# Performance work log

Measured on AMD Instinct MI355X. Metric: run time of the kernel, lower is better.

Reference implementation:

```python
import math
import jax, jax.numpy as jnp
import numpy as np

B = 32            # batch
C = 64            # prior_feat_channels == fc_hidden_dim
MID = 48          # ROIGather mid_channels
P = 192           # num_priors
S = 36            # sample_points
N_OFFSETS = 72
N_STRIPS = 71
IMG_W, IMG_H = 800, 320
SCALE_FACTOR = 20.0
RH, RW = 10, 25   # FeatureResize target size

SAMPLE_X_IDX = np.floor(np.linspace(0.0, 1.0, S) * N_STRIPS).astype(np.int32)
PRIOR_FEAT_YS = (1.0 - SAMPLE_X_IDX.astype(np.float32) / N_STRIPS)[::-1].copy()
PRIOR_YS = np.linspace(1.0, 0.0, N_OFFSETS, dtype=np.float32)
SX = jnp.asarray(SAMPLE_X_IDX)

def _make_priors():
    pri = np.zeros((P, 6 + N_OFFSETS), np.float32)
    pri[:, 0], pri[:, 1], pri[:, 2] = 0.1, 0.9, 0.5
    pri[:, 3], pri[:, 4], pri[:, 5] = 0.1, 0.0, 50.0
    pri[:, 6:] = ((np.arange(P, dtype=np.float32) + 0.5) / P)[:, None]
    return jnp.asarray(pri)

def _conv1d(x, w, pad):
    # x (N, Cin, L), w (Cout, Cin, K); cross-correlation like torch
    return jax.lax.conv_general_dilated(x, w, (1,), [(pad, pad)], dimension_numbers=('NCH', 'OIH', 'NCH'))

def _resize_nearest(x):
    # F.interpolate(mode='nearest') to (RH, RW), then flatten(2)
    b, c, h, w = x.shape
    hi = (jnp.arange(RH) * h) // RH
    wi = (jnp.arange(RW) * w) // RW
    return x[:, :, hi[:, None], wi[None, :]].reshape(b, c, RH * RW)

def _grid_sample(feat, gx, gy):
    # bilinear, align_corners=True, zeros padding; feat (B,C,H,W), gx/gy (B,P,S)
    b, c, h, w = feat.shape
    ix = (gx + 1.0) * 0.5 * (w - 1)
    iy = (gy + 1.0) * 0.5 * (h - 1)
    x0, y0 = jnp.floor(ix), jnp.floor(iy)
    fflat = feat.reshape(b, c, h * w)
    def corner(xc, yc, wt):
        valid = (xc >= 0) & (xc <= w - 1) & (yc >= 0) & (yc <= h - 1)
        xi = jnp.clip(xc, 0, w - 1).astype(jnp.int32)
        yi = jnp.clip(yc, 0, h - 1).astype(jnp.int32)
        idx = (yi * w + xi).reshape(b, 1, -1)
        v = jnp.take_along_axis(fflat, jnp.broadcast_to(idx, (b, c, idx.shape[-1])), axis=2)
        return v.reshape(b, c, *xc.shape[1:]) * (wt * valid)[:, None]
    return (corner(x0, y0, (x0 + 1 - ix) * (y0 + 1 - iy))
            + corner(x0 + 1, y0, (ix - x0) * (y0 + 1 - iy))
            + corner(x0, y0 + 1, (x0 + 1 - ix) * (iy - y0))
            + corner(x0 + 1, y0 + 1, (ix - x0) * (iy - y0)))


def setup_inputs() -> dict:
    key = jax.random.key(0)
    ks = iter(jax.random.split(key, 64))
    def rn(shape, s=0.05):
        return jax.random.normal(next(ks), shape, jnp.float32) * s
    def ru(shape):
        return jax.random.uniform(next(ks), shape, jnp.float32, 0.5, 1.5)
    return dict(
        feat_s8=rn((B, C, 40, 100), 1.0), feat_s16=rn((B, C, 20, 50), 1.0), feat_s32=rn((B, C, 10, 25), 1.0),
        rg_conv_w=rn((3, MID, C, 9)), rg_conv_scale=ru((3, MID)), rg_conv_bias=rn((3, MID)),
        catconv0_w=rn((C, MID, 9)), catconv1_w=rn((C, 2 * MID, 9)), catconv2_w=rn((C, 3 * MID, 9)),
        catconv_scale=ru((3, C)), catconv_bias=rn((3, C)),
        fc_w=rn((C, C * S)), fc_b=rn((C,)), ln_gamma=ru((C,)), ln_beta=rn((C,)),
        fkey_w=rn((C, C)), fkey_scale=ru((C,)), fkey_bias=rn((C,)),
        fvalue_w=rn((C, C)), fvalue_b=rn((C,)),
        fquery_w=ru((P,)), fquery_b=rn((P,)), attn_w_scale=rn((P,)), attn_w_bias=rn((P,)),
        cls_w1=rn((C, C)), cls_b1=rn((C,)), cls_w2=rn((C, C)), cls_b2=rn((C,)),
        reg_w1=rn((C, C)), reg_b1=rn((C,)), reg_w2=rn((C, C)), reg_b2=rn((C,)),
        cls_head_w=rn((2, C)), cls_head_b=rn((2,)),
        reg_head_w=rn((N_OFFSETS + 4, C)), reg_head_b=rn((N_OFFSETS + 4,)),
        cat_w1=rn((C, C)), cat_b1=rn((C,)), cat_w2=rn((C, C)), cat_b2=rn((C,)),
        prototypes=rn((15, C), 0.01),
        attr_w1=rn((C, C)), attr_b1=rn((C,)), attr_w2=rn((C, C)), attr_b2=rn((C,)),
        attr_head_w=rn((4, C)), attr_head_b=rn((4,)),
    )


def reference(feat_s8, feat_s16, feat_s32, rg_conv_w, rg_conv_scale, rg_conv_bias,
              catconv0_w, catconv1_w, catconv2_w, catconv_scale, catconv_bias,
              fc_w, fc_b, ln_gamma, ln_beta, fkey_w, fkey_scale, fkey_bias,
              fvalue_w, fvalue_b, fquery_w, fquery_b, attn_w_scale, attn_w_bias,
              cls_w1, cls_b1, cls_w2, cls_b2, reg_w1, reg_b1, reg_w2, reg_b2,
              cls_head_w, cls_head_b, reg_head_w, reg_head_b,
              cat_w1, cat_b1, cat_w2, cat_b2, prototypes,
              attr_w1, attr_b1, attr_w2, attr_b2, attr_head_w, attr_head_b):
    relu = jax.nn.relu
    catconv_ws = (catconv0_w, catconv1_w, catconv2_w)
    batch_features = [feat_s32, feat_s16, feat_s8]  # features[-3:] reversed
    priors = jnp.broadcast_to(_make_priors()[None], (B, P, 6 + N_OFFSETS))
    pofm = priors[..., 6 + SX]
    prior_ys = jnp.asarray(PRIOR_YS)
    gy_row = jnp.asarray(PRIOR_FEAT_YS) * 2.0 - 1.0  # (S,)

    roi_stages, predictions, ff_last = [], None, None
    for stage in range(3):
        feat = batch_features[stage]
        prior_xs = jnp.flip(pofm, axis=2)            # (B,P,S)
        gx = prior_xs * 2.0 - 1.0
        gy = jnp.broadcast_to(gy_row[None, None, :], gx.shape)
        pooled = _grid_sample(feat, gx, gy)          # (B,C,P,S)
        pooled = pooled.transpose(0, 2, 1, 3).reshape(B * P, C, S)
        roi_stages.append(pooled)

        # ROIGather.roi_fea: per-stage (9,1) convs (BN folded to scale/bias) + cat conv
        feats = [relu(_conv1d(roi_stages[i], rg_conv_w[i], 4)
                      * rg_conv_scale[i][None, :, None] + rg_conv_bias[i][None, :, None])
                 for i in range(stage + 1)]
        cat_feat = jnp.concatenate(feats, axis=1)
        roi = relu(_conv1d(cat_feat, catconv_ws[stage], 4)
                   * catconv_scale[stage][None, :, None] + catconv_bias[stage][None, :, None])
        # fc + LayerNorm + relu
        roi = roi.reshape(B * P, C * S) @ fc_w.T + fc_b
        mu = roi.mean(-1, keepdims=True)
        var = ((roi - mu) ** 2).mean(-1, keepdims=True)
        roi = (roi - mu) * jax.lax.rsqrt(var + 1e-5) * ln_gamma + ln_beta
        roi = relu(roi).reshape(B, P, C)

        # cross-attention with (nearest-)resized feature map
        key_map = relu(jnp.einsum('bchw,oc->bohw', feat, fkey_w)
                       * fkey_scale[None, :, None, None] + fkey_bias[None, :, None, None])
        key_map = _resize_nearest(key_map)                     # (B,C,N)
        val_map = jnp.einsum('bchw,oc->bohw', feat, fvalue_w) + fvalue_b[None, :, None, None]
        val_map = _resize_nearest(val_map).transpose(0, 2, 1)  # (B,N,C)
        query = relu(roi * fquery_w[None, :, None] + fquery_b[None, :, None])  # grouped 1x1 conv1d
        sim = jax.nn.softmax(jnp.einsum('bpc,bcn->bpn', query, key_map) * (C ** -0.5), axis=-1)
        context = jnp.einsum('bpn,bnc->bpc', sim, val_map)
        context = context * attn_w_scale[None, :, None] + attn_w_bias[None, :, None]
        roi = roi + context

        # faithful to source: view(P,B,C).permute(1,0,2) memory reinterpretation
        ff = roi.reshape(P, B, C).transpose(1, 0, 2).reshape(B * P, C)
        ff_last = ff

        cls_f = relu(ff @ cls_w1.T + cls_b1)
        cls_f = relu(cls_f @ cls_w2.T + cls_b2)
        reg_f = relu(ff @ reg_w1.T + reg_b1)
        reg_f = relu(reg_f @ reg_w2.T + reg_b2)
        cls_logits = (cls_f @ cls_head_w.T + cls_head_b).reshape(B, P, 2)
        reg = (reg_f @ reg_head_w.T + reg_head_b).reshape(B, P, N_OFFSETS + 4)

        p2 = priors[:, :, 2] + reg[:, :, 0]
        p3 = priors[:, :, 3] + reg[:, :, 1]
        p4 = priors[:, :, 4] + reg[:, :, 2]
        p5 = reg[:, :, 3]
        geom = (p3[:, :, None] * (IMG_W - 1)
                + (1.0 - prior_ys[None, None, :] - p2[:, :, None]) * IMG_H
                / jnp.tan(p4[:, :, None] * math.pi + 1e-5)) / (IMG_W - 1)
        lines = jnp.concatenate([cls_logits, p2[..., None], p3[..., None],
                                 p4[..., None], p5[..., None], geom], axis=-1)
        predictions = lines.at[..., 6:].add(reg[:, :, 4:])
        if stage != 2:
            priors = jax.lax.stop_gradient(lines)
            pofm = priors[..., 6 + SX]

    # prototype-based cosine category head (final stage features)
    cat_f = relu(ff_last @ cat_w1.T + cat_b1)
    cat_f = relu(cat_f @ cat_w2.T + cat_b2)
    cat_n = cat_f / jnp.maximum(jnp.linalg.norm(cat_f, axis=-1, keepdims=True), 1e-12)
    proto_n = prototypes / jnp.maximum(jnp.linalg.norm(prototypes, axis=-1, keepdims=True), 1e-12)
    category = (cat_n @ proto_n.T * SCALE_FACTOR).reshape(B, P, -1)
    # left-right attribute head
    attr_f = relu(ff_last @ attr_w1.T + attr_b1)
    attr_f = relu(attr_f @ attr_w2.T + attr_b2)
    attribute = (attr_f @ attr_head_w.T + attr_head_b).reshape(B, P, -1)
    return predictions, category, attribute
```

## Files before the change

kernel.cpp:

```cpp
#include <hip/hip_runtime.h>
#include <math.h>

#define PPRI 192
#define NB   32
#define NS   36
#define BP   6144
#define NPIX 250
#define FPI  3.14159265358979323846f

typedef _Float16 f16x8 __attribute__((ext_vector_type(8)));
typedef float f32x4  __attribute__((ext_vector_type(4)));

__device__ inline short f2h(float x) {
    _Float16 h = (_Float16)x;
    return *(short*)&h;
}
__device__ inline float h2f(short s) {
    _Float16 h = *(_Float16*)&s;
    return (float)h;
}
__device__ inline void splith(float x, short& h, short& l) {
    h = f2h(x); l = f2h(x - h2f(h));
}

// ... 14 lines not shown
                       const float* __restrict__ attr_w1, const float* __restrict__ attr_w2,
                       const float* __restrict__ reg_head_w, const float* __restrict__ cls_head_w,
                       const float* __restrict__ attr_head_w) {
    int i = blockIdx.x * 256 + threadIdx.x;
    if (i < BP * NS) {
        int p = (i / NS) % PPRI;
        pofm[i] = ((float)p + 0.5f) / 192.0f;
    }
    if (i < BP) {
        p234[3*i+0] = 0.5f; p234[3*i+1] = 0.1f; p234[3*i+2] = 0.0f;
    }
    if (i < 64 * 2304) {
        int o = i / 2304, k = i % 2304;
        int s = k >> 6, oc = k & 63;
        short h, l; splith(fc_w[o * 2304 + oc * 36 + s], h, l);
        fcBh[i] = h; fcBl[i] = l;
    }
    if (i < 82944) {
        int st = i / 27648, r = i % 27648;
        int k = r / 3072, r2 = r % 3072;
        int oc = r2 / 64, ic = r2 & 63;
        short h, l; splith(rg_w[((st*48 + oc)*64 + ic)*9 + k], h, l);
        rgWh[i] = h; rgWl[i] = l;
    }
    if (i < 184320) {
        int st, base, icw; const float* w;
        if (i < 36864)      { st = 0; base = 0;     icw = 64;  w = cw0; }
        else if (i < 92160) { st = 1; base = 36864; icw = 96;  w = cw1; }
        else                { st = 2; base = 92160; icw = 160; w = cw2; }
        int r = i - base;
        int k = r / (64*icw), r2 = r % (64*icw);
        int oc = r2 / icw, icp = r2 % icw;
        int IC = 48 * (st + 1);
        float wv = (icp < IC) ? w[(oc*IC + icp)*9 + k] : 0.f;
        short h, l; splith(wv, h, l);
        catWh[i] = h; catWl[i] = l;
    }
    if (i < 32768) {
        int m = i >> 12, r2 = i & 4095, c = r2 >> 6, o = r2 & 63;
        const float* Ws[8] = {reg_w1, reg_w2, cls_w1, cls_w2, cat_w1, cat_w2, attr_w1, attr_w2};
        hT[i] = Ws[m][o*64 + c];
    }
    if (i < 76*64) {
        int c = i / 76, o = i % 76;
        rhwT[c*76 + o] = reg_head_w[o*64 + c];
    }
    if (i < 128) {
        int c = i >> 1, o = i & 1;
        chwT[c*2 + o] = cls_head_w[o*64 + c];
    }
    if (i < 256) {
        int c = i >> 2, o = i & 3;
        ahwT[c*4 + o] = attr_head_w[o*64 + c];
    }
    if (i < 960) {
        int c = i / 15, p = i % 15;
        float ss = 0.f;
        for (int j = 0; j < 64; ++j) { float v = protos[p*64 + j]; ss += v*v; }
        float nrm = fmaxf(sqrtf(ss), 1e-12f);
        protoNT[c*15 + p] = protos[p*64 + c] / nrm;
    }
}

__global__ __launch_bounds__(256) void k_transpose(const float* __restrict__ in,
                                                   float* __restrict__ outT, int HW) {
    __shared__ float t[64][65];
    int b = blockIdx.y;
    int hw0 = blockIdx.x * 64;
    int tx = threadIdx.x & 63, ty = threadIdx.x >> 6;
    const float* ib = in + (size_t)b * 64 * HW;
    for (int c = ty; c < 64; c += 4) {
        int hw = hw0 + tx;
        t[c][tx] = (hw < HW) ? ib[(size_t)c * HW + hw] : 0.f;
    }
    __syncthreads();
    float* ob = outT + (size_t)b * HW * 64;
    for (int r = ty; r < 64; r += 4) {
        int hw = hw0 + r;
        if (hw < HW) ob[(size_t)hw * 64 + tx] = t[tx][r];
    }
}

#define RGWP 80
template<bool SPL>
__global__ __launch_bounds__(192) void k_rgfused(
        const float* __restrict__ featT, int H, int W,
        const float* __restrict__ pofm,
        const short* __restrict__ Wh, const short* __restrict__ Wl,
        const float* __restrict__ scale, const float* __restrict__ bias,
        short* __restrict__ outH, short* __restrict__ outL) {
    constexpr int STG = (SPL ? 2 : 1) * 37 * RGWP;
    constexpr int RED = 9 * 256 * 2;
    constexpr int SMS = (STG > RED) ? STG : RED;
    __shared__ short sm[SMS];
    int tid = threadIdx.x;
    int row = blockIdx.x;
    int wv = tid >> 6, lane = tid & 63;
    int b = row / PPRI;
    float myPof = (lane < 36) ? pofm[row * 36 + lane] : 0.f;
    const float* fb = featT + (size_t)b * H * W * 64;
    for (int si = 0; si < 12; ++si) {
        int s = wv * 12 + si;
        float px = __shfl(myPof, 35 - s);
        px = fminf(fmaxf(px, -1e6f), 1e6f);
        float pfy = (s == 0) ? 0.0f : ((float)(2*s+1) / 71.0f);
        float ix = px  * (float)(W - 1);
        float iy = pfy * (float)(H - 1);
        float x0f = floorf(ix), y0f = floorf(iy);
        float fx = ix - x0f, fy = iy - y0f;
        float vx0 = (x0f >= 0.f     && x0f     <= (float)(W-1)) ? 1.f : 0.f;
        float vx1 = (x0f+1.f >= 0.f && x0f+1.f <= (float)(W-1)) ? 1.f : 0.f;
        float vy0 = (y0f >= 0.f     && y0f     <= (float)(H-1)) ? 1.f : 0.f;
        float vy1 = (y0f+1.f >= 0.f && y0f+1.f <= (float)(H-1)) ? 1.f : 0.f;
        int x0 = min(max((int)x0f, 0), W-1);
        int x1 = min(max((int)x0f + 1, 0), W-1);
        int y0 = min(max((int)y0f, 0), H-1);
        int y1 = min(max((int)y0f + 1, 0), H-1);
        float w00 = (1.f-fx)*(1.f-fy)*vx0*vy0, w10 = fx*(1.f-fy)*vx1*vy0;
        float w01 = (1.f-fx)*fy*vx0*vy1,       w11 = fx*fy*vx1*vy1;
        float v = w00 * fb[(size_t)(y0*W+x0)*64 + lane]
                + w10 * fb[(size_t)(y0*W+x1)*64 + lane]
                + w01 * fb[(size_t)(y1*W+x0)*64 + lane]
                + w11 * fb[(size_t)(y1*W+x1)*64 + lane];
        int di = (s*RGWP + lane) ^ (((s >> 2) & 1) << 3);
        if (SPL) {
            short h, l; splith(v, h, l);
            sm[di] = h;
            sm[37*RGWP + di] = l;
        } else {
            sm[di] = f2h(v);
        }
    }
    if (wv == 0) {
        int di = (36*RGWP + lane) ^ 8;
        sm[di] = 0;
        if (SPL) sm[37*RGWP + di] = 0;
    }
    __syncthreads();
    int lr = lane & 15, kg = lane >> 4;
    const short* shb = sm;
    const short* slb = sm + 37*RGWP;
    f32x4 acc[3][3] = {};
    #pragma unroll
    for (int ssh = 0; ssh < 3; ++ssh) {
        int sh = wv*3 + ssh;
        int sr0 = lr + sh - 4;
        int ar0 = ((unsigned)sr0 < 36u) ? sr0 : 36;
        int ar1 = 16 + lr + sh - 4;
        int sr2 = 32 + lr + sh - 4;
        int ar2 = ((unsigned)sr2 < 36u) ? sr2 : 36;
        int rb0 = ar0*RGWP, rs0 = ((ar0 >> 2) & 1) << 3;
        int rb1 = ar1*RGWP, rs1 = ((ar1 >> 2) & 1) << 3;
        int rb2 = ar2*RGWP, rs2 = ((ar2 >> 2) & 1) << 3;
        #pragma unroll
        for (int kc = 0; kc < 2; ++kc) {
            int icb = kc*32 + kg*8;
            int d0 = (rb0 + icb) ^ rs0;
            int d1 = (rb1 + icb) ^ rs1;
            int d2 = (rb2 + icb) ^ rs2;
            f16x8 ah[3] = { *(const f16x8*)(shb + d0), *(const f16x8*)(shb + d1),
                            *(const f16x8*)(shb + d2) };
            const short* wbh = Wh + (size_t)(sh*48)*64 + icb;
            f16x8 bh[3];
            #pragma unroll
            for (int nt = 0; nt < 3; ++nt) bh[nt] = *(const f16x8*)(wbh + (nt*16 + lr)*64);
            if (SPL) {
                f16x8 al[3] = { *(const f16x8*)(slb + d0), *(const f16x8*)(slb + d1),
                                *(const f16x8*)(slb + d2) };
                const short* wbl = Wl + (size_t)(sh*48)*64 + icb;
                f16x8 bl[3];
                #pragma unroll
                for (int nt = 0; nt < 3; ++nt) bl[nt] = *(const f16x8*)(wbl + (nt*16 + lr)*64);
                #pragma unroll
                for (int nt = 0; nt < 3; ++nt)
                    #pragma unroll
                    for (int mt = 0; mt < 3; ++mt)
                        acc[mt][nt] = __builtin_amdgcn_mfma_f32_16x16x32_f16(ah[mt], bh[nt], acc[mt][nt], 0,0,0);
                #pragma unroll
                for (int nt = 0; nt < 3; ++nt)
                    #pragma unroll
                    for (int mt = 0; mt < 3; ++mt)
                        acc[mt][nt] = __builtin_amdgcn_mfma_f32_16x16x32_f16(ah[mt], bl[nt], acc[mt][nt], 0,0,0);
                #pragma unroll
                for (int nt = 0; nt < 3; ++nt)
                    #pragma unroll
                    for (int mt = 0; mt < 3; ++mt)
                        acc[mt][nt] = __builtin_amdgcn_mfma_f32_16x16x32_f16(al[mt], bh[nt], acc[mt][nt], 0,0,0);
            } else {
                #pragma unroll
                for (int nt = 0; nt < 3; ++nt)
                    #pragma unroll
                    for (int mt = 0; mt < 3; ++mt)
                        acc[mt][nt] = __builtin_amdgcn_mfma_f32_16x16x32_f16(ah[mt], bh[nt], acc[mt][nt], 0,0,0);
            }
        }
    }
    __syncthreads();
    float* red = (float*)sm;
    if (wv == 2) {
        #pragma unroll
        for (int mt = 0; mt < 3; ++mt)
            #pragma unroll
            for (int nt = 0; nt < 3; ++nt)
                *(f32x4*)(red + ((size_t)(mt*3 + nt))*256 + lane*4) = acc[mt][nt];
    }
    __syncthreads();
    if (wv == 1) {
        #pragma unroll
        for (int mt = 0; mt < 3; ++mt)
            #pragma unroll
            for (int nt = 0; nt < 3; ++nt) {
                f32x4* p = (f32x4*)(red + ((size_t)(mt*3 + nt))*256 + lane*4);
                *p = *p + acc[mt][nt];
            }
    }
    __syncthreads();
    if (wv == 0) {
        #pragma unroll
        for (int nt = 0; nt < 3; ++nt) {
            int oc = nt*16 + lr;
            float sc = scale[oc], bi = bias[oc];
            #pragma unroll
            for (int mt = 0; mt < 3; ++mt) {
                f32x4 a = acc[mt][nt] + *(const f32x4*)(red + ((size_t)(mt*3 + nt))*256 + lane*4);
                #pragma unroll
                for (int i = 0; i < 4; ++i) {
                    int s = mt*16 + kg*4 + i;
                    if (s < 36) {
                        float v = fmaxf(a[i]*sc + bi, 0.f);
                        if (SPL) {
                            short h, l; splith(v, h, l);
                            outH[(size_t)row*36*48 + s*48 + oc] = h;
                            outL[(size_t)row*36*48 + s*48 + oc] = l;
                        } else {
                            outH[(size_t)row*36*48 + s*48 + oc] = f2h(v);
                        }
                    }
                }
            }
        }
    }
}

template<int NC, int NT, int BW, int WP, int ICR, bool SPL>
__global__ __launch_bounds__(192) void k_catconv(
        const short* __restrict__ Xh, const short* __restrict__ Xl,
        const short* __restrict__ Wh, const short* __restrict__ Wl,
        const float* __restrict__ scale, const float* __restrict__ bias,
        short* __restrict__ outH, short* __restrict__ outL) {
    constexpr int icw = NC * 32;
    constexpr int CH  = icw / 8;
    constexpr int STG = (SPL ? 2 : 1) * 37 * WP;
    constexpr int RED = 3 * NT * 256 * 2;
    constexpr int SMS = (STG > RED) ? STG : RED;
    __shared__ short sm[SMS];
    int tid = threadIdx.x;
    int row = blockIdx.x;
    for (int idx = tid; idx < 37*CH; idx += 192) {
        int pos = idx / CH, c0 = (idx % CH) << 3;
        f16x8 h = {}, l = {};
        if (pos < 36 && c0 < ICR) {
            int sidx = c0 / BW, cc = c0 % BW;
            size_t src = ((size_t)(sidx*BP + row)*36 + pos)*BW + cc;
            h = *(const f16x8*)(Xh + src);
            if (SPL) l = *(const f16x8*)(Xl + src);
        }
        int di = (pos*WP + c0) ^ (((pos >> 2) & 1) << 3);
        *(f16x8*)(sm + di) = h;
        if (SPL) *(f16x8*)(sm + 37*WP + di) = l;
    }
    __syncthreads();
    int wv = tid >> 6, lane = tid & 63;
    int lr = lane & 15, kg = lane >> 4;
    const short* shb = sm;
    const short* slb = sm + 37*WP;
    f32x4 acc[3][NT] = {};
    #pragma unroll
    for (int ssh = 0; ssh < 3; ++ssh) {
        int sh = wv*3 + ssh;
        int sr0 = lr + sh - 4;
        int ar0 = ((unsigned)sr0 < 36u) ? sr0 : 36;
        int ar1 = 16 + lr + sh - 4;
        int sr2 = 32 + lr + sh - 4;
        int ar2 = ((unsigned)sr2 < 36u) ? sr2 : 36;
        int rb0 = ar0*WP, rs0 = ((ar0 >> 2) & 1) << 3;
        int rb1 = ar1*WP, rs1 = ((ar1 >> 2) & 1) << 3;
        int rb2 = ar2*WP, rs2 = ((ar2 >> 2) & 1) << 3;
        #pragma unroll
        for (int kc = 0; kc < NC; ++kc) {
            int icb = kc*32 + kg*8;
            int d0 = (rb0 + icb) ^ rs0;
            int d1 = (rb1 + icb) ^ rs1;
            int d2 = (rb2 + icb) ^ rs2;
            f16x8 ah[3] = { *(const f16x8*)(shb + d0), *(const f16x8*)(shb + d1),
                            *(const f16x8*)(shb + d2) };
            const short* wbh = Wh + (size_t)(sh*NT*16)*icw + icb;
            f16x8 bh[NT];
            #pragma unroll
            for (int nt = 0; nt < NT; ++nt) bh[nt] = *(const f16x8*)(wbh + (nt*16 + lr)*icw);
            if (SPL) {
                f16x8 al[3] = { *(const f16x8*)(slb + d0), *(const f16x8*)(slb + d1),
                                *(const f16x8*)(slb + d2) };
                const short* wbl = Wl + (size_t)(sh*NT*16)*icw + icb;
                f16x8 bl[NT];
                #pragma unroll
                for (int nt = 0; nt < NT; ++nt) bl[nt] = *(const f16x8*)(wbl + (nt*16 + lr)*icw);
                #pragma unroll
                for (int nt = 0; nt < NT; ++nt)
                    #pragma unroll
                    for (int mt = 0; mt < 3; ++mt)
                        acc[mt][nt] = __builtin_amdgcn_mfma_f32_16x16x32_f16(ah[mt], bh[nt], acc[mt][nt], 0,0,0);
                #pragma unroll
                for (int nt = 0; nt < NT; ++nt)
                    #pragma unroll
                    for (int mt = 0; mt < 3; ++mt)
                        acc[mt][nt] = __builtin_amdgcn_mfma_f32_16x16x32_f16(ah[mt], bl[nt], acc[mt][nt], 0,0,0);
                #pragma unroll
                for (int nt = 0; nt < NT; ++nt)
                    #pragma unroll
                    for (int mt = 0; mt < 3; ++mt)
                        acc[mt][nt] = __builtin_amdgcn_mfma_f32_16x16x32_f16(al[mt], bh[nt], acc[mt][nt], 0,0,0);
            } else {
                #pragma unroll
                for (int nt = 0; nt < NT; ++nt)
                    #pragma unroll
                    for (int mt = 0; mt < 3; ++mt)
                        acc[mt][nt] = __builtin_amdgcn_mfma_f32_16x16x32_f16(ah[mt], bh[nt], acc[mt][nt], 0,0,0);
            }
        }
    }
    __syncthreads();
    float* red = (float*)sm;
    if (wv == 2) {
        #pragma unroll
        for (int mt = 0; mt < 3; ++mt)
            #pragma unroll
            for (int nt = 0; nt < NT; ++nt)
                *(f32x4*)(red + ((size_t)(mt*NT + nt))*256 + lane*4) = acc[mt][nt];
    }
    __syncthreads();
    if (wv == 1) {
        #pragma unroll
        for (int mt = 0; mt < 3; ++mt)
            #pragma unroll
            for (int nt = 0; nt < NT; ++nt) {
                f32x4* p = (f32x4*)(red + ((size_t)(mt*NT + nt))*256 + lane*4);
                *p = *p + acc[mt][nt];
            }
    }
    __syncthreads();
    if (wv == 0) {
        constexpr int OC = NT * 16;
        #pragma unroll
        for (int nt = 0; nt < NT; ++nt) {
            int oc = nt*16 + lr;
            float sc = scale[oc], bi = bias[oc];
            #pragma unroll
            for (int mt = 0; mt < 3; ++mt) {
                f32x4 a = acc[mt][nt] + *(const f32x4*)(red + ((size_t)(mt*NT + nt))*256 + lane*4);
                #pragma unroll
                for (int i = 0; i < 4; ++i) {
                    int s = mt*16 + kg*4 + i;
                    if (s < 36) {
                        float v = fmaxf(a[i]*sc + bi, 0.f);
                        short h, l; splith(v, h, l);
                        outH[(size_t)row*36*OC + s*OC + oc] = h;
                        outL[(size_t)row*36*OC + s*OC + oc] = l;
                    }
                }
            }
        }
    }
}

__global__ __launch_bounds__(256) void k_fc_mfma(
        const short* __restrict__ Ah, const short* __restrict__ Al,
        const short* __restrict__ Bh, const short* __restrict__ Bl,
        const float* __restrict__ fcb,
        const float* __restrict__ gamma, const float* __restrict__ beta,
        float* __restrict__ roi) {
    __shared__ float red[3 * 4 * 256];
    __shared__ float lnb[16][65];
    int tid = threadIdx.x;
    int wv = tid >> 6, lane = tid & 63;
    int lr = lane & 15, kg = lane >> 4;
    int row0 = blockIdx.x * 16;
    f32x4 acc[4] = {};
    for (int kk = 0; kk < 18; ++kk) {
        int k = (wv*18 + kk)*32 + kg*8;
        size_t ar = (size_t)(row0 + lr)*2304 + k;
        f16x8 ah = *(const f16x8*)(Ah + ar);
        f16x8 al = *(const f16x8*)(Al + ar);
        f16x8 bh[4], bl[4];
        #pragma unroll
        for (int nt = 0; nt < 4; ++nt) {
            size_t br = (size_t)(nt*16 + lr)*2304 + k;
            bh[nt] = *(const f16x8*)(Bh + br);
            bl[nt] = *(const f16x8*)(Bl + br);
        }
        #pragma unroll
        for (int nt = 0; nt < 4; ++nt)
            acc[nt] = __builtin_amdgcn_mfma_f32_16x16x32_f16(ah, bh[nt], acc[nt], 0,0,0);
        #pragma unroll
        for (int nt = 0; nt < 4; ++nt)
            acc[nt] = __builtin_amdgcn_mfma_f32_16x16x32_f16(ah, bl[nt], acc[nt], 0,0,0);
        #pragma unroll
        for (int nt = 0; nt < 4; ++nt)
            acc[nt] = __builtin_amdgcn_mfma_f32_16x16x32_f16(al, bh[nt], acc[nt], 0,0,0);
    }
    if (wv > 0) {
        #pragma unroll
        for (int nt = 0; nt < 4; ++nt)
            *(f32x4*)(red + ((size_t)((wv-1)*4 + nt))*256 + lane*4) = acc[nt];
    }
    __syncthreads();
    if (wv == 0) {
        #pragma unroll
        for (int nt = 0; nt < 4; ++nt) {
            f32x4 a = acc[nt]
                    + *(const f32x4*)(red + ((size_t)(0*4 + nt))*256 + lane*4)
                    + *(const f32x4*)(red + ((size_t)(1*4 + nt))*256 + lane*4)
                    + *(const f32x4*)(red + ((size_t)(2*4 + nt))*256 + lane*4);
            #pragma unroll
            for (int i = 0; i < 4; ++i)
                lnb[kg*4 + i][nt*16 + lr] = a[i];
        }
    }
    __syncthreads();
    #pragma unroll
    for (int rr = 0; rr < 4; ++rr) {
        int r = wv*4 + rr;
        float y = lnb[r][lane] + fcb[lane];
        float sum = y;
        #pragma unroll
        for (int off = 32; off > 0; off >>= 1) sum += __shfl_xor(sum, off);
        float mu = sum * (1.f/64.f);
        float d = y - mu;
        float vs = d * d;
        #pragma unroll
        for (int off = 32; off > 0; off >>= 1) vs += __shfl_xor(vs, off);
        float var = vs * (1.f/64.f);
        float outv = d * (1.0f / sqrtf(var + 1e-5f)) * gamma[lane] + beta[lane];
        roi[(size_t)(row0 + r)*64 + lane] = fmaxf(outv, 0.f);
    }
}

__global__ __launch_bounds__(64) void k_keyval(const float* __restrict__ featT, int H, int W,
        const float* __restrict__ kw, const float* __restrict__ ks, const float* __restrict__ kb,
        const float* __restrict__ vw, const float* __restrict__ vb,
        float* __restrict__ keymap, float* __restrict__ valmap) {
// ... 193 lines not shown
    const float* rg_conv_w     = (const float*)d_in[3];
    const float* rg_conv_scale = (const float*)d_in[4];
    const float* rg_conv_bias  = (const float*)d_in[5];
    const float* catconv_w[3]  = {(const float*)d_in[6], (const float*)d_in[7], (const float*)d_in[8]};
    const float* catconv_scale = (const float*)d_in[9];
    const float* catconv_bias  = (const float*)d_in[10];
    const float* fc_w = (const float*)d_in[11];
    const float* fc_b = (const float*)d_in[12];
    const float* ln_gamma = (const float*)d_in[13];
    const float* ln_beta  = (const float*)d_in[14];
    const float* fkey_w = (const float*)d_in[15];
    const float* fkey_scale = (const float*)d_in[16];
    const float* fkey_bias  = (const float*)d_in[17];
    const float* fvalue_w = (const float*)d_in[18];
    const float* fvalue_b = (const float*)d_in[19];
    const float* fquery_w = (const float*)d_in[20];
    const float* fquery_b = (const float*)d_in[21];
    const float* attn_w_scale = (const float*)d_in[22];
    const float* attn_w_bias  = (const float*)d_in[23];
    const float* cls_w1 = (const float*)d_in[24];
    const float* cls_b1 = (const float*)d_in[25];
    const float* cls_w2 = (const float*)d_in[26];
    const float* cls_b2 = (const float*)d_in[27];
    const float* reg_w1 = (const float*)d_in[28];
    const float* reg_b1 = (const float*)d_in[29];
    const float* reg_w2 = (const float*)d_in[30];
    const float* reg_b2 = (const float*)d_in[31];
    const float* cls_head_w = (const float*)d_in[32];
    const float* cls_head_b = (const float*)d_in[33];
    const float* reg_head_w = (const float*)d_in[34];
    const float* reg_head_b = (const float*)d_in[35];
    const float* cat_w1 = (const float*)d_in[36];
    const float* cat_b1 = (const float*)d_in[37];
    const float* cat_w2 = (const float*)d_in[38];
    const float* cat_b2 = (const float*)d_in[39];
    const float* prototypes = (const float*)d_in[40];
    const float* attr_w1 = (const float*)d_in[41];
    const float* attr_b1 = (const float*)d_in[42];
    const float* attr_w2 = (const float*)d_in[43];
    const float* attr_b2 = (const float*)d_in[44];
    const float* attr_head_w = (const float*)d_in[45];
    const float* attr_head_b = (const float*)d_in[46];

    float* ws = (float*)d_ws;
    float* pofm   = ws;
    float* p234   = ws + 221184;
    short* fcBh   = (short*)(ws + 240576);
    short* fcBl   = (short*)(ws + 314304);
    float* roi    = ws + 388032;
    float* keymap = ws + 781248;
    float* valmap = ws + 1293248;
    short* catHh  = (short*)(ws + 1805248);
    short* catHl  = (short*)(ws + 8883136);
    float* featT  = ws + 15961024;
    short* rgCh   = (short*)(ws + 30116800);
    short* rgCl   = (short*)(ws + 46042048);
    short* rgWh   = (short*)(ws + 61967296);
    short* rgWl   = (short*)(ws + 62008768);
    short* catWh  = (short*)(ws + 62050240);
    short* catWl  = (short*)(ws + 62142400);
    float* hT      = ws + 62234560;
    float* rhwT    = ws + 62267328;
    float* chwT    = ws + 62272192;
    float* ahwT    = ws + 62272320;
    float* protoNT = ws + 62272576;

    float* out = (float*)d_out;

    k_init<<<864, 256, 0, stream>>>(pofm, p234, fcBh, fcBl, fc_w, prototypes,
                                    rgWh, rgWl, rg_conv_w, catWh, catWl,
                                    catconv_w[0], catconv_w[1], catconv_w[2],
                                    hT, rhwT, chwT, ahwT, protoNT,
                                    reg_w1, reg_w2, cls_w1, cls_w2,
                                    cat_w1, cat_w2, attr_w1, attr_w2,
                                    reg_head_w, cls_head_w, attr_head_w);

    const float* feats[3] = {feat_s32, feat_s16, feat_s8};
    const int Hs[3] = {10, 20, 40}, Wstg[3] = {25, 50, 100};
    const int catbase[3] = {0, 36864, 92160};

    for (int st = 0; st < 3; ++st) {
        int HW = Hs[st] * Wstg[st];
        k_transpose<<<dim3((HW + 63)/64, NB), 256, 0, stream>>>(feats[st], featT, HW);
        if (st < 2)
            k_rgfused<true><<<BP, 192, 0, stream>>>(featT, Hs[st], Wstg[st], pofm,
                                                    rgWh + st*27648, rgWl + st*27648,
                                                    rg_conv_scale + st*48, rg_conv_bias + st*48,
                                                    rgCh + (size_t)st*BP*1728, rgCl + (size_t)st*BP*1728);
        else
            k_rgfused<false><<<BP, 192, 0, stream>>>(featT, Hs[st], Wstg[st], pofm,
                                                     rgWh + st*27648, rgWl + st*27648,
                                                     rg_conv_scale + st*48, rg_conv_bias + st*48,
                                                     rgCh + (size_t)st*BP*1728, rgCl + (size_t)st*BP*1728);
        if (st == 0)
            k_catconv<2,4,48,80,48,true><<<BP, 192, 0, stream>>>(
                    rgCh, rgCl, catWh + catbase[0], catWl + catbase[0],
                    catconv_scale, catconv_bias, catHh, catHl);
        else if (st == 1)
            k_catconv<3,4,48,112,96,true><<<BP, 192, 0, stream>>>(
                    rgCh, rgCl, catWh + catbase[1], catWl + catbase[1],
                    catconv_scale + 64, catconv_bias + 64, catHh, catHl);
        else
            k_catconv<5,4,48,176,144,false><<<BP, 192, 0, stream>>>(
                    rgCh, rgCl, catWh + catbase[2], catWl + catbase[2],
                    catconv_scale + 128, catconv_bias + 128, catHh, catHl);
        k_fc_mfma<<<384, 256, 0, stream>>>(catHh, catHl, fcBh, fcBl,
                                           fc_b, ln_gamma, ln_beta, roi);
        k_keyval<<<NB*NPIX, 64, 0, stream>>>(featT, Hs[st], Wstg[st],
                                             fkey_w, fkey_scale, fkey_bias,
                                             fvalue_w, fvalue_b, keymap, valmap);
        k_attn<<<BP, 256, 0, stream>>>(roi, keymap, valmap, fquery_w, fquery_b,
                                       attn_w_scale, attn_w_bias);
        k_head<<<BP, 128, 0, stream>>>(st, p234, pofm, roi,
                                       hT + 0, reg_b1, hT + 4096, reg_b2, rhwT, reg_head_b,
                                       hT + 8192, cls_b1, hT + 12288, cls_b2, chwT, cls_head_b,
                                       out);
    }
    k_catattr<<<BP, 64, 0, stream>>>(roi, hT + 16384, cat_b1, hT + 20480, cat_b2, protoNT,
                                     hT + 24576, attr_b1, hT + 28672, attr_b2,
                                     ahwT, attr_head_b, out);
}
```

Baseline: 1.037 ms.

## Fuse ROI gather conv with concatenated stage conv in one kernel

Merges the per-stage gather-and-conv kernel with the following concatenation conv kernel, so each row's freshly computed gather features are written straight into the shared staging buffer of the second convolution. Only earlier stages' features are re-read from global memory, and the last stage no longer writes its gather output to global. This removes one launch per stage and a global round trip. In exchange shared memory use per block grows because separate buffers for both convolutions and the reduction now coexist, which may lower occupancy.

```diff
diff --git a/kernel.cpp b/kernel.cpp
--- a/kernel.cpp
+++ b/kernel.cpp
@@ -120,17 +120,25 @@
 }
 
 #define RGWP 80
-template<bool SPL>
-__global__ __launch_bounds__(192) void k_rgfused(
+template<int NC, int NT, int BW, int WP, int ICR, int OWN0, bool SPL, bool WRG>
+__global__ __launch_bounds__(192) void k_rgcat(
         const float* __restrict__ featT, int H, int W,
         const float* __restrict__ pofm,
-        const short* __restrict__ Wh, const short* __restrict__ Wl,
-        const float* __restrict__ scale, const float* __restrict__ bias,
+        const short* __restrict__ rWh, const short* __restrict__ rWl,
+        const float* __restrict__ rsc, const float* __restrict__ rbi,
+        const short* __restrict__ cWh, const short* __restrict__ cWl,
+        const float* __restrict__ csc, const float* __restrict__ cbi,
+        short* __restrict__ rgHout, short* __restrict__ rgLout,
+        const short* __restrict__ Xh, const short* __restrict__ Xl,
         short* __restrict__ outH, short* __restrict__ outL) {
-    constexpr int STG = (SPL ? 2 : 1) * 37 * RGWP;
-    constexpr int RED = 9 * 256 * 2;
-    constexpr int SMS = (STG > RED) ? STG : RED;
-    __shared__ short sm[SMS];
+    constexpr int icw  = NC * 32;
+    constexpr int CH   = icw / 8;
+    constexpr int ARW  = (SPL ? 2 : 1) * 37 * RGWP;
+    constexpr int BRW  = (SPL ? 2 : 1) * 37 * WP;
+    constexpr int REDS = (3*NT*512 > 9*512) ? 3*NT*512 : 9*512;
+    __shared__ short smA[ARW];
+    __shared__ short smB[BRW];
+    __shared__ short smR[REDS];
     int tid = threadIdx.x;
     int row = blockIdx.x;
     int wv = tid >> 6, lane = tid & 63;
@@ -163,139 +171,21 @@
         int di = (s*RGWP + lane) ^ (((s >> 2) & 1) << 3);
         if (SPL) {
             short h, l; splith(v, h, l);
-            sm[di] = h;
-            sm[37*RGWP + di] = l;
+            smA[di] = h;
+            smA[37*RGWP + di] = l;
         } else {
-            sm[di] = f2h(v);
+            smA[di] = f2h(v);
         }
     }
     if (wv == 0) {
         int di = (36*RGWP + lane) ^ 8;
-        sm[di] = 0;
-        if (SPL) sm[37*RGWP + di] = 0;
-    }
-    __syncthreads();
-    int lr = lane & 15, kg = lane >> 4;
-    const short* shb = sm;
-    const short* slb = sm + 37*RGWP;
-    f32x4 acc[3][3] = {};
-    #pragma unroll
-    for (int ssh = 0; ssh < 3; ++ssh) {
-        int sh = wv*3 + ssh;
-        int sr0 = lr + sh - 4;
-        int ar0 = ((unsigned)sr0 < 36u) ? sr0 : 36;
-        int ar1 = 16 + lr + sh - 4;
-        int sr2 = 32 + lr + sh - 4;
-        int ar2 = ((unsigned)sr2 < 36u) ? sr2 : 36;
-        int rb0 = ar0*RGWP, rs0 = ((ar0 >> 2) & 1) << 3;
-        int rb1 = ar1*RGWP, rs1 = ((ar1 >> 2) & 1) << 3;
-        int rb2 = ar2*RGWP, rs2 = ((ar2 >> 2) & 1) << 3;
-        #pragma unroll
-        for (int kc = 0; kc < 2; ++kc) {
-            int icb = kc*32 + kg*8;
-            int d0 = (rb0 + icb) ^ rs0;
-            int d1 = (rb1 + icb) ^ rs1;
-            int d2 = (rb2 + icb) ^ rs2;
-            f16x8 ah[3] = { *(const f16x8*)(shb + d0), *(const f16x8*)(shb + d1),
-                            *(const f16x8*)(shb + d2) };
-            const short* wbh = Wh + (size_t)(sh*48)*64 + icb;
-            f16x8 bh[3];
-            #pragma unroll
-            for (int nt = 0; nt < 3; ++nt) bh[nt] = *(const f16x8*)(wbh + (nt*16 + lr)*64);
-            if (SPL) {
-                f16x8 al[3] = { *(const f16x8*)(slb + d0), *(const f16x8*)(slb + d1),
-                                *(const f16x8*)(slb + d2) };
-                const short* wbl = Wl + (size_t)(sh*48)*64 + icb;
-                f16x8 bl[3];
-                #pragma unroll
-                for (int nt = 0; nt < 3; ++nt) bl[nt] = *(const f16x8*)(wbl + (nt*16 + lr)*64);
-                #pragma unroll
-                for (int nt = 0; nt < 3; ++nt)
-                    #pragma unroll
-                    for (int mt = 0; mt < 3; ++mt)
-                        acc[mt][nt] = __builtin_amdgcn_mfma_f32_16x16x32_f16(ah[mt], bh[nt], acc[mt][nt], 0,0,0);
-                #pragma unroll
-                for (int nt = 0; nt < 3; ++nt)
-                    #pragma unroll
-                    for (int mt = 0; mt < 3; ++mt)
-                        acc[mt][nt] = __builtin_amdgcn_mfma_f32_16x16x32_f16(ah[mt], bl[nt], acc[mt][nt], 0,0,0);
-                #pragma unroll
-                for (int nt = 0; nt < 3; ++nt)
-                    #pragma unroll
-                    for (int mt = 0; mt < 3; ++mt)
-                        acc[mt][nt] = __builtin_amdgcn_mfma_f32_16x16x32_f16(al[mt], bh[nt], acc[mt][nt], 0,0,0);
-            } else {
-                #pragma unroll
-                for (int nt = 0; nt < 3; ++nt)
-                    #pragma unroll
-                    for (int mt = 0; mt < 3; ++mt)
-                        acc[mt][nt] = __builtin_amdgcn_mfma_f32_16x16x32_f16(ah[mt], bh[nt], acc[mt][nt], 0,0,0);
-            }
-        }
-    }
-    __syncthreads();
-    float* red = (float*)sm;
-    if (wv == 2) {
-        #pragma unroll
-        for (int mt = 0; mt < 3; ++mt)
-            #pragma unroll
-            for (int nt = 0; nt < 3; ++nt)
-                *(f32x4*)(red + ((size_t)(mt*3 + nt))*256 + lane*4) = acc[mt][nt];
-    }
-    __syncthreads();
-    if (wv == 1) {
-        #pragma unroll
-        for (int mt = 0; mt < 3; ++mt)
-            #pragma unroll
-            for (int nt = 0; nt < 3; ++nt) {
-                f32x4* p = (f32x4*)(red + ((size_t)(mt*3 + nt))*256 + lane*4);
-                *p = *p + acc[mt][nt];
-            }
-    }
-    __syncthreads();
-    if (wv == 0) {
-        #pragma unroll
-        for (int nt = 0; nt < 3; ++nt) {
-            int oc = nt*16 + lr;
-            float sc = scale[oc], bi = bias[oc];
-            #pragma unroll
-            for (int mt = 0; mt < 3; ++mt) {
-                f32x4 a = acc[mt][nt] + *(const f32x4*)(red + ((size_t)(mt*3 + nt))*256 + lane*4);
-                #pragma unroll
-                for (int i = 0; i < 4; ++i) {
-                    int s = mt*16 + kg*4 + i;
-                    if (s < 36) {
-                        float v = fmaxf(a[i]*sc + bi, 0.f);
-                        if (SPL) {
-                            short h, l; splith(v, h, l);
-                            outH[(size_t)row*36*48 + s*48 + oc] = h;
-                            outL[(size_t)row*36*48 + s*48 + oc] = l;
-                        } else {
-                            outH[(size_t)row*36*48 + s*48 + oc] = f2h(v);
-                        }
-                    }
-                }
-            }
-        }
-    }
-}
-
-template<int NC, int NT, int BW, int WP, int ICR, bool SPL>
-__global__ __launch_bounds__(192) void k_catconv(
-        const short* __restrict__ Xh, const short* __restrict__ Xl,
-        const short* __restrict__ Wh, const short* __restrict__ Wl,
-        const float* __restrict__ scale, const float* __restrict__ bias,
-        short* __restrict__ outH, short* __restrict__ outL) {
-    constexpr int icw = NC * 32;
-    constexpr int CH  = icw / 8;
-    constexpr int STG = (SPL ? 2 : 1) * 37 * WP;
-    constexpr int RED = 3 * NT * 256 * 2;
-    constexpr int SMS = (STG > RED) ? STG : RED;
-    __shared__ short sm[SMS];
-    int tid = threadIdx.x;
-    int row = blockIdx.x;
+        smA[di] = 0;
+        if (SPL) smA[37*RGWP + di] = 0;
+    }
     for (int idx = tid; idx < 37*CH; idx += 192) {
         int pos = idx / CH, c0 = (idx % CH) << 3;
+        bool own = (c0 >= OWN0) && (c0 < OWN0 + 48);
+        if (own && pos < 36) continue;
         f16x8 h = {}, l = {};
         if (pos < 36 && c0 < ICR) {
             int sidx = c0 / BW, cc = c0 % BW;
@@ -304,106 +194,219 @@
             if (SPL) l = *(const f16x8*)(Xl + src);
         }
         int di = (pos*WP + c0) ^ (((pos >> 2) & 1) << 3);
-        *(f16x8*)(sm + di) = h;
-        if (SPL) *(f16x8*)(sm + 37*WP + di) = l;
-    }
-    __syncthreads();
-    int wv = tid >> 6, lane = tid & 63;
+        *(f16x8*)(smB + di) = h;
+        if (SPL) *(f16x8*)(smB + 37*WP + di) = l;
+    }
+    __syncthreads();
     int lr = lane & 15, kg = lane >> 4;
-    const short* shb = sm;
-    const short* slb = sm + 37*WP;
-    f32x4 acc[3][NT] = {};
-    #pragma unroll
-    for (int ssh = 0; ssh < 3; ++ssh) {
-        int sh = wv*3 + ssh;
-        int sr0 = lr + sh - 4;
-        int ar0 = ((unsigned)sr0 < 36u) ? sr0 : 36;
-        int ar1 = 16 + lr + sh - 4;
-        int sr2 = 32 + lr + sh - 4;
-        int ar2 = ((unsigned)sr2 < 36u) ? sr2 : 36;
-        int rb0 = ar0*WP, rs0 = ((ar0 >> 2) & 1) << 3;
-        int rb1 = ar1*WP, rs1 = ((ar1 >> 2) & 1) << 3;
-        int rb2 = ar2*WP, rs2 = ((ar2 >> 2) & 1) << 3;
-        #pragma unroll
-        for (int kc = 0; kc < NC; ++kc) {
-            int icb = kc*32 + kg*8;
-            int d0 = (rb0 + icb) ^ rs0;
-            int d1 = (rb1 + icb) ^ rs1;
-            int d2 = (rb2 + icb) ^ rs2;
-            f16x8 ah[3] = { *(const f16x8*)(shb + d0), *(const f16x8*)(shb + d1),
-                            *(const f16x8*)(shb + d2) };
-            const short* wbh = Wh + (size_t)(sh*NT*16)*icw + icb;
-            f16x8 bh[NT];
+    {
+        const short* shb = smA;
+        const short* slb = smA + 37*RGWP;
+        f32x4 acc[3][3] = {};
+        #pragma unroll
+        for (int ssh = 0; ssh < 3; ++ssh) {
+            int sh = wv*3 + ssh;
+            int sr0 = lr + sh - 4;
+            int ar0 = ((unsigned)sr0 < 36u) ? sr0 : 36;
+            int ar1 = 16 + lr + sh - 4;
+            int sr2 = 32 + lr + sh - 4;
+            int ar2 = ((unsigned)sr2 < 36u) ? sr2 : 36;
+            int rb0 = ar0*RGWP, rs0 = ((ar0 >> 2) & 1) << 3;
+            int rb1 = ar1*RGWP, rs1 = ((ar1 >> 2) & 1) << 3;
+            int rb2 = ar2*RGWP, rs2 = ((ar2 >> 2) & 1) << 3;
             #pragma unroll
-            for (int nt = 0; nt < NT; ++nt) bh[nt] = *(const f16x8*)(wbh + (nt*16 + lr)*icw);
-            if (SPL) {
-                f16x8 al[3] = { *(const f16x8*)(slb + d0), *(const f16x8*)(slb + d1),
-                                *(const f16x8*)(slb + d2) };
-                const short* wbl = Wl + (size_t)(sh*NT*16)*icw + icb;
-                f16x8 bl[NT];
+            for (int kc = 0; kc < 2; ++kc) {
+                int icb = kc*32 + kg*8;
+                int d0 = (rb0 + icb) ^ rs0;
+                int d1 = (rb1 + icb) ^ rs1;
+                int d2 = (rb2 + icb) ^ rs2;
+                f16x8 ah[3] = { *(const f16x8*)(shb + d0), *(const f16x8*)(shb + d1),
+                                *(const f16x8*)(shb + d2) };
+                const short* wbh = rWh + (size_t)(sh*48)*64 + icb;
+                f16x8 bh[3];
                 #pragma unroll
-                for (int nt = 0; nt < NT; ++nt) bl[nt] = *(const f16x8*)(wbl + (nt*16 + lr)*icw);
+                for (int nt = 0; nt < 3; ++nt) bh[nt] = *(const f16x8*)(wbh + (nt*16 + lr)*64);
+                if (SPL) {
+                    f16x8 al[3] = { *(const f16x8*)(slb + d0), *(const f16x8*)(slb + d1),
+                                    *(const f16x8*)(slb + d2) };
+                    const short* wbl = rWl + (size_t)(sh*48)*64 + icb;
+                    f16x8 bl[3];
+                    #pragma unroll
+                    for (int nt = 0; nt < 3; ++nt) bl[nt] = *(const f16x8*)(wbl + (nt*16 + lr)*64);
+                    #pragma unroll
+                    for (int nt = 0; nt < 3; ++nt)
+                        #pragma unroll
+                        for (int mt = 0; mt < 3; ++mt)
+                            acc[mt][nt] = __builtin_amdgcn_mfma_f32_16x16x32_f16(ah[mt], bh[nt], acc[mt][nt], 0,0,0);
+                    #pragma unroll
+                    for (int nt = 0; nt < 3; ++nt)
+                        #pragma unroll
+                        for (int mt = 0; mt < 3; ++mt)
+                            acc[mt][nt] = __builtin_amdgcn_mfma_f32_16x16x32_f16(ah[mt], bl[nt], acc[mt][nt], 0,0,0);
+                    #pragma unroll
+                    for (int nt = 0; nt < 3; ++nt)
+                        #pragma unroll
+                        for (int mt = 0; mt < 3; ++mt)
+                            acc[mt][nt] = __builtin_amdgcn_mfma_f32_16x16x32_f16(al[mt], bh[nt], acc[mt][nt], 0,0,0);
+                } else {
+                    #pragma unroll
+                    for (int nt = 0; nt < 3; ++nt)
+                        #pragma unroll
+                        for (int mt = 0; mt < 3; ++mt)
+                            acc[mt][nt] = __builtin_amdgcn_mfma_f32_16x16x32_f16(ah[mt], bh[nt], acc[mt][nt], 0,0,0);
+                }
+            }
+        }
+        __syncthreads();
+        float* red = (float*)smR;
+        if (wv == 2) {
+            #pragma unroll
+            for (int mt = 0; mt < 3; ++mt)
+                #pragma unroll
+                for (int nt = 0; nt < 3; ++nt)
+                    *(f32x4*)(red + ((size_t)(mt*3 + nt))*256 + lane*4) = acc[mt][nt];
+        }
+        __syncthreads();
+        if (wv == 1) {
+            #pragma unroll
+            for (int mt = 0; mt < 3; ++mt)
+                #pragma unroll
+                for (int nt = 0; nt < 3; ++nt) {
+                    f32x4* p = (f32x4*)(red + ((size_t)(mt*3 + nt))*256 + lane*4);
+                    *p = *p + acc[mt][nt];
+                }
+        }
+        __syncthreads();
+        if (wv == 0) {
+            #pragma unroll
+            for (int nt = 0; nt < 3; ++nt) {
+                int oc = nt*16 + lr;
+                float sc = rsc[oc], bi = rbi[oc];
+                #pragma unroll
+                for (int mt = 0; mt < 3; ++mt) {
+                    f32x4 a = acc[mt][nt] + *(const f32x4*)(red + ((size_t)(mt*3 + nt))*256 + lane*4);
+                    #pragma unroll
+                    for (int i = 0; i < 4; ++i) {
+                        int s = mt*16 + kg*4 + i;
+                        if (s < 36) {
+                            float v = fmaxf(a[i]*sc + bi, 0.f);
+                            int di = (s*WP + OWN0 + oc) ^ (((s >> 2) & 1) << 3);
+                            if (SPL) {
+                                short h, l; splith(v, h, l);
+                                smB[di] = h;
+                                smB[37*WP + di] = l;
+                                if (WRG) {
+                                    rgHout[(size_t)row*36*48 + s*48 + oc] = h;
+                                    rgLout[(size_t)row*36*48 + s*48 + oc] = l;
+                                }
+                            } else {
+                                short h = f2h(v);
+                                smB[di] = h;
+                                if (WRG) rgHout[(size_t)row*36*48 + s*48 + oc] = h;
+                            }
+                        }
+                    }
+                }
+            }
+        }
+    }
+    __syncthreads();
+    {
+        const short* shb = smB;
+        const short* slb = smB + 37*WP;
+        f32x4 acc[3][NT] = {};
+        #pragma unroll
+        for (int ssh = 0; ssh < 3; ++ssh) {
+            int sh = wv*3 + ssh;
+            int sr0 = lr + sh - 4;
+            int ar0 = ((unsigned)sr0 < 36u) ? sr0 : 36;
+            int ar1 = 16 + lr + sh - 4;
+            int sr2 = 32 + lr + sh - 4;
+            int ar2 = ((unsigned)sr2 < 36u) ? sr2 : 36;
+            int rb0 = ar0*WP, rs0 = ((ar0 >> 2) & 1) << 3;
+            int rb1 = ar1*WP, rs1 = ((ar1 >> 2) & 1) << 3;
+            int rb2 = ar2*WP, rs2 = ((ar2 >> 2) & 1) << 3;
+            #pragma unroll
+            for (int kc = 0; kc < NC; ++kc) {
+                int icb = kc*32 + kg*8;
+                int d0 = (rb0 + icb) ^ rs0;
+                int d1 = (rb1 + icb) ^ rs1;
+                int d2 = (rb2 + icb) ^ rs2;
+                f16x8 ah[3] = { *(const f16x8*)(shb + d0), *(const f16x8*)(shb + d1),
+                                *(const f16x8*)(shb + d2) };
+                const short* wbh = cWh + (size_t)(sh*NT*16)*icw + icb;
+                f16x8 bh[NT];
+                #pragma unroll
+                for (int nt = 0; nt < NT; ++nt) bh[nt] = *(const f16x8*)(wbh + (nt*16 + lr)*icw);
+                if (SPL) {
+                    f16x8 al[3] = { *(const f16x8*)(slb + d0), *(const f16x8*)(slb + d1),
+                                    *(const f16x8*)(slb + d2) };
+                    const short* wbl = cWl + (size_t)(sh*NT*16)*icw + icb;
+                    f16x8 bl[NT];
+                    #pragma unroll
+                    for (int nt = 0; nt < NT; ++nt) bl[nt] = *(const f16x8*)(wbl + (nt*16 + lr)*icw);
+                    #pragma unroll
+                    for (int nt = 0; nt < NT; ++nt)
+                        #pragma unroll
+                        for (int mt = 0; mt < 3; ++mt)
+                            acc[mt][nt] = __builtin_amdgcn_mfma_f32_16x16x32_f16(ah[mt], bh[nt], acc[mt][nt], 0,0,0);
+                    #pragma unroll
+                    for (int nt = 0; nt < NT; ++nt)
+                        #pragma unroll
+                        for (int mt = 0; mt < 3; ++mt)
+                            acc[mt][nt] = __builtin_amdgcn_mfma_f32_16x16x32_f16(ah[mt], bl[nt], acc[mt][nt], 0,0,0);
+                    #pragma unroll
+                    for (int nt = 0; nt < NT; ++nt)
+                        #pragma unroll
+                        for (int mt = 0; mt < 3; ++mt)
+                            acc[mt][nt] = __builtin_amdgcn_mfma_f32_16x16x32_f16(al[mt], bh[nt], acc[mt][nt], 0,0,0);
+                } else {
+                    #pragma unroll
+                    for (int nt = 0; nt < NT; ++nt)
+                        #pragma unroll
+                        for (int mt = 0; mt < 3; ++mt)
+                            acc[mt][nt] = __builtin_amdgcn_mfma_f32_16x16x32_f16(ah[mt], bh[nt], acc[mt][nt], 0,0,0);
+                }
+            }
+        }
+        __syncthreads();
+        float* red = (float*)smR;
+        if (wv == 2) {
+            #pragma unroll
+            for (int mt = 0; mt < 3; ++mt)
                 #pragma unroll
                 for (int nt = 0; nt < NT; ++nt)
-                    #pragma unroll
-                    for (int mt = 0; mt < 3; ++mt)
-                        acc[mt][nt] = __builtin_amdgcn_mfma_f32_16x16x32_f16(ah[mt], bh[nt], acc[mt][nt], 0,0,0);
+                    *(f32x4*)(red + ((size_t)(mt*NT + nt))*256 + lane*4) = acc[mt][nt];
+        }
+        __syncthreads();
+        if (wv == 1) {
+            #pragma unroll
+            for (int mt = 0; mt < 3; ++mt)
                 #pragma unroll
-                for (int nt = 0; nt < NT; ++nt)
-                    #pragma unroll
-                    for (int mt = 0; mt < 3; ++mt)
-                        acc[mt][nt] = __builtin_amdgcn_mfma_f32_16x16x32_f16(ah[mt], bl[nt], acc[mt][nt], 0,0,0);
-                #pragma unroll
-                for (int nt = 0; nt < NT; ++nt)
-                    #pragma unroll
-                    for (int mt = 0; mt < 3; ++mt)
-                        acc[mt][nt] = __builtin_amdgcn_mfma_f32_16x16x32_f16(al[mt], bh[nt], acc[mt][nt], 0,0,0);
-            } else {
-                #pragma unroll
-                for (int nt = 0; nt < NT; ++nt)
-                    #pragma unroll
-                    for (int mt = 0; mt < 3; ++mt)
-                        acc[mt][nt] = __builtin_amdgcn_mfma_f32_16x16x32_f16(ah[mt], bh[nt], acc[mt][nt], 0,0,0);
-            }
-        }
-    }
-    __syncthreads();
-    float* red = (float*)sm;
-    if (wv == 2) {
-        #pragma unroll
-        for (int mt = 0; mt < 3; ++mt)
-            #pragma unroll
-            for (int nt = 0; nt < NT; ++nt)
-                *(f32x4*)(red + ((size_t)(mt*NT + nt))*256 + lane*4) = acc[mt][nt];
-    }
-    __syncthreads();
-    if (wv == 1) {
-        #pragma unroll
-        for (int mt = 0; mt < 3; ++mt)
+                for (int nt = 0; nt < NT; ++nt) {
+                    f32x4* p = (f32x4*)(red + ((size_t)(mt*NT + nt))*256 + lane*4);
+                    *p = *p + acc[mt][nt];
+                }
+        }
+        __syncthreads();
+        if (wv == 0) {
+            constexpr int OC = NT * 16;
             #pragma unroll
             for (int nt = 0; nt < NT; ++nt) {
-                f32x4* p = (f32x4*)(red + ((size_t)(mt*NT + nt))*256 + lane*4);
-                *p = *p + acc[mt][nt];
-            }
-    }
-    __syncthreads();
-    if (wv == 0) {
-        constexpr int OC = NT * 16;
-        #pragma unroll
-        for (int nt = 0; nt < NT; ++nt) {
-            int oc = nt*16 + lr;
-            float sc = scale[oc], bi = bias[oc];
-            #pragma unroll
-            for (int mt = 0; mt < 3; ++mt) {
-                f32x4 a = acc[mt][nt] + *(const f32x4*)(red + ((size_t)(mt*NT + nt))*256 + lane*4);
+                int oc = nt*16 + lr;
+                float sc = csc[oc], bi = cbi[oc];
                 #pragma unroll
-                for (int i = 0; i < 4; ++i) {
-                    int s = mt*16 + kg*4 + i;
-                    if (s < 36) {
-                        float v = fmaxf(a[i]*sc + bi, 0.f);
-                        short h, l; splith(v, h, l);
-                        outH[(size_t)row*36*OC + s*OC + oc] = h;
-                        outL[(size_t)row*36*OC + s*OC + oc] = l;
+                for (int mt = 0; mt < 3; ++mt) {
+                    f32x4 a = acc[mt][nt] + *(const f32x4*)(red + ((size_t)(mt*NT + nt))*256 + lane*4);
+                    #pragma unroll
+                    for (int i = 0; i < 4; ++i) {
+                        int s = mt*16 + kg*4 + i;
+                        if (s < 36) {
+                            float v = fmaxf(a[i]*sc + bi, 0.f);
+                            short h, l; splith(v, h, l);
+                            outH[(size_t)row*36*OC + s*OC + oc] = h;
+                            outL[(size_t)row*36*OC + s*OC + oc] = l;
+                        }
                     }
                 }
             }
@@ -763,28 +766,24 @@
     for (int st = 0; st < 3; ++st) {
         int HW = Hs[st] * Wstg[st];
         k_transpose<<<dim3((HW + 63)/64, NB), 256, 0, stream>>>(feats[st], featT, HW);
-        if (st < 2)
-            k_rgfused<true><<<BP, 192, 0, stream>>>(featT, Hs[st], Wstg[st], pofm,
-                                                    rgWh + st*27648, rgWl + st*27648,
-                                                    rg_conv_scale + st*48, rg_conv_bias + st*48,
-                                                    rgCh + (size_t)st*BP*1728, rgCl + (size_t)st*BP*1728);
+        if (st == 0)
+            k_rgcat<2,4,48,80,48,0,true,true><<<BP, 192, 0, stream>>>(
+                    featT, Hs[0], Wstg[0], pofm,
+                    rgWh, rgWl, rg_conv_scale, rg_conv_bias,
+                    catWh + catbase[0], catWl + catbase[0], catconv_scale, catconv_bias,
+                    rgCh, rgCl, rgCh, rgCl, catHh, catHl);
+        else if (st == 1)
+            k_rgcat<3,4,48,112,96,48,true,true><<<BP, 192, 0, stream>>>(
+                    featT, Hs[1], Wstg[1], pofm,
+                    rgWh + 27648, rgWl + 27648, rg_conv_scale + 48, rg_conv_bias + 48,
+                    catWh + catbase[1], catWl + catbase[1], catconv_scale + 64, catconv_bias + 64,
+                    rgCh + (size_t)BP*1728, rgCl + (size_t)BP*1728, rgCh, rgCl, catHh, catHl);
         else
-            k_rgfused<false><<<BP, 192, 0, stream>>>(featT, Hs[st], Wstg[st], pofm,
-                                                     rgWh + st*27648, rgWl + st*27648,
-                                                     rg_conv_scale + st*48, rg_conv_bias + st*48,
-                                                     rgCh + (size_t)st*BP*1728, rgCl + (size_t)st*BP*1728);
-        if (st == 0)
-            k_catconv<2,4,48,80,48,true><<<BP, 192, 0, stream>>>(
-                    rgCh, rgCl, catWh + catbase[0], catWl + catbase[0],
-                    catconv_scale, catconv_bias, catHh, catHl);
-        else if (st == 1)
-            k_catconv<3,4,48,112,96,true><<<BP, 192, 0, stream>>>(
-                    rgCh, rgCl, catWh + catbase[1], catWl + catbase[1],
-                    catconv_scale + 64, catconv_bias + 64, catHh, catHl);
-        else
-            k_catconv<5,4,48,176,144,false><<<BP, 192, 0, stream>>>(
-                    rgCh, rgCl, catWh + catbase[2], catWl + catbase[2],
-                    catconv_scale + 128, catconv_bias + 128, catHh, catHl);
+            k_rgcat<5,4,48,176,144,96,false,false><<<BP, 192, 0, stream>>>(
+                    featT, Hs[2], Wstg[2], pofm,
+                    rgWh + 2*27648, rgWl + 2*27648, rg_conv_scale + 96, rg_conv_bias + 96,
+                    catWh + catbase[2], catWl + catbase[2], catconv_scale + 128, catconv_bias + 128,
+                    nullptr, nullptr, rgCh, rgCl, catHh, catHl);
         k_fc_mfma<<<384, 256, 0, stream>>>(catHh, catHl, fcBh, fcBl,
                                            fc_b, ln_gamma, ln_beta, roi);
         k_keyval<<<NB*NPIX, 64, 0, stream>>>(featT, Hs[st], Wstg[st],
```

After: 1.122 ms. +8.2%, slower.
